# Kernel tuning notes

Hardware: AMD Instinct MI355X
Metric: run time of the kernel (lower is better)

Reference implementation:

```python
import jax, jax.numpy as jnp
import numpy as np

B, H, KVH, S, D, DPE = 16, 128, 1, 4096, 512, 64


def setup_inputs() -> dict:
    key = jax.random.key(0)
    k1, k2, k3, k4 = jax.random.split(key, 4)
    return {
        "q": jax.random.normal(k1, (B, H, D), dtype=jnp.float32),
        "q_pe": jax.random.normal(k2, (B, H, DPE), dtype=jnp.float32),
        "k": jax.random.normal(k3, (B, S, KVH, D), dtype=jnp.float32),
        "k_pe": jax.random.normal(k4, (B, S, KVH, DPE), dtype=jnp.float32),
    }


def reference(q, q_pe, k, k_pe):
    # MLA decode: latent KV cache (k serves as both key-nope part and value),
    # separate rotary-positional path (q_pe, k_pe). kv_head_num groups heads.
    b, h, d = q.shape
    kvh = k.shape[2]
    g = h // kvh  # query heads per latent kv head
    dpe = q_pe.shape[-1]
    scale = 1.0 / jnp.sqrt(jnp.asarray(d + dpe, dtype=q.dtype))
    qg = q.reshape(b, kvh, g, d)          # [b, kvh, g, d]
    qg_pe = q_pe.reshape(b, kvh, g, dpe)  # [b, kvh, g, dpe]
    # scores[b, kvh, g, s] = q . k_latent + q_pe . k_pe
    scores = (jnp.einsum('bkgd,bskd->bkgs', qg, k)
              + jnp.einsum('bkgp,bskp->bkgs', qg_pe, k_pe)) * scale
    p = jax.nn.softmax(scores, axis=-1)
    # value = latent cache (nope dim part)
    out = jnp.einsum('bkgs,bskd->bkgd', p, k)
    return out.reshape(b, h, d)
```

## Files before the change

kernel.cpp:

```cpp
#include <hip/hip_runtime.h>
#include <hip/hip_bf16.h>

typedef __attribute__((ext_vector_type(4))) float  f32x4;
typedef __attribute__((ext_vector_type(8))) short  s16x8;

#define NB_    16
#define NH_    128
#define NS_    4096
#define ND_    512
#define NDPE_  64
#define NCHUNK 16
#define CHUNK_ 256
#define TS_    32
#define NSUB_  8
#define NT_    512

#define KROW_S 584
#define VROW_S 40

#define KBUF_OFF 0
#define VBUF_OFF (TS_ * KROW_S * 2)
#define PBUF_OFF (VBUF_OFF + ND_ * VROW_S * 2)
#define SMEM_BYTES (PBUF_OFF + 8 * 16 * VROW_S * 2)

#define CL2 0.06011229337037348f

__device__ __forceinline__ unsigned short f2bf(float f) {
    unsigned u = __float_as_uint(f);
    u += 0x7FFFu + ((u >> 16) & 1u);
    return (unsigned short)(u >> 16);
}

__global__ __launch_bounds__(NT_, 2) void mla_attn(
    const float* __restrict__ q, const float* __restrict__ q_pe,
    const float* __restrict__ k, const float* __restrict__ k_pe,
    unsigned short* __restrict__ opart, float* __restrict__ mlbuf)
{
    extern __shared__ char smem[];
    unsigned short* kbuf = (unsigned short*)(smem + KBUF_OFF);
    unsigned short* vbuf = (unsigned short*)(smem + VBUF_OFF);
    unsigned short* pbuf = (unsigned short*)(smem + PBUF_OFF);

    const int chunk = blockIdx.x, b = blockIdx.y;
    const int tid = threadIdx.x;
    const int wv  = tid >> 6;
    const int l   = tid & 63;
    const int l16 = l & 15;
    const int lq  = l >> 4;

    f32x4 acc[32];
    #pragma unroll
    for (int i = 0; i < 32; ++i) acc[i] = (f32x4)0.0f;
    float m2[4]   = {-1e30f, -1e30f, -1e30f, -1e30f};
    float lsum[4] = {0.f, 0.f, 0.f, 0.f};

    const int sl   = tid >> 4;
    const int ln16 = tid & 15;

    const float* qrow   = q    + (size_t)(b*NH_ + wv*16 + l16) * ND_;
    const float* qperow = q_pe + (size_t)(b*NH_ + wv*16 + l16) * NDPE_;

    unsigned short* prow = pbuf + wv * 16 * VROW_S;

    for (int t = 0; t < NSUB_; ++t) {
        {
            const int sg = chunk*CHUNK_ + t*TS_ + sl;
            const float* krow   = k    + (size_t)(b*NS_ + sg) * ND_;
            const float* kperow = k_pe + (size_t)(b*NS_ + sg) * NDPE_;
            #pragma unroll
            for (int i = 0; i < 9; ++i) {
                const int d0 = ln16*4 + i*64;
                f32x4 v;
                if (i < 8) v = *(const f32x4*)(krow + d0);
                else       v = *(const f32x4*)(kperow + (d0 - ND_));
                const unsigned short b0 = f2bf(v.x), b1 = f2bf(v.y),
                                     b2 = f2bf(v.z), b3 = f2bf(v.w);
                unsigned* kp = (unsigned*)&kbuf[sl*KROW_S + d0];
                kp[0] = (unsigned)b0 | ((unsigned)b1 << 16);
                kp[1] = (unsigned)b2 | ((unsigned)b3 << 16);
                if (i < 8) {
                    vbuf[(d0+0)*VROW_S + sl] = b0;
                    vbuf[(d0+1)*VROW_S + sl] = b1;
                    vbuf[(d0+2)*VROW_S + sl] = b2;
                    vbuf[(d0+3)*VROW_S + sl] = b3;
                }
            }
        }
        __syncthreads();

        f32x4 sc0 = (f32x4)0.0f, sc1 = (f32x4)0.0f;
        #pragma unroll
        for (int kk = 0; kk < 18; ++kk) {
            const int d0 = kk*32 + lq*8;
            f32x4 qa, qb;
            if (kk < 16) {
                qa = *(const f32x4*)(qrow + d0);
                qb = *(const f32x4*)(qrow + d0 + 4);
            } else {
                qa = *(const f32x4*)(qperow + (d0 - ND_));
                qb = *(const f32x4*)(qperow + (d0 - ND_ + 4));
            }
            s16x8 af;
            {
                union { unsigned u[4]; s16x8 s; } w;
                w.u[0] = (unsigned)f2bf(qa.x) | ((unsigned)f2bf(qa.y) << 16);
                w.u[1] = (unsigned)f2bf(qa.z) | ((unsigned)f2bf(qa.w) << 16);
                w.u[2] = (unsigned)f2bf(qb.x) | ((unsigned)f2bf(qb.y) << 16);
                w.u[3] = (unsigned)f2bf(qb.z) | ((unsigned)f2bf(qb.w) << 16);
                af = w.s;
            }
            const s16x8 bf0 = *(const s16x8*)&kbuf[(l16     )*KROW_S + d0];
            const s16x8 bf1 = *(const s16x8*)&kbuf[(l16 + 16)*KROW_S + d0];
            sc0 = __builtin_amdgcn_mfma_f32_16x16x32_bf16(af, bf0, sc0, 0, 0, 0);
            sc1 = __builtin_amdgcn_mfma_f32_16x16x32_bf16(af, bf1, sc1, 0, 0, 0);
        }

        float alpha[4];
        #pragma unroll
        for (int r = 0; r < 4; ++r) {
            float mx = fmaxf(sc0[r], sc1[r]);
            mx = fmaxf(mx, __shfl_xor(mx, 1));
            mx = fmaxf(mx, __shfl_xor(mx, 2));
            mx = fmaxf(mx, __shfl_xor(mx, 4));
            mx = fmaxf(mx, __shfl_xor(mx, 8));
            const float mn = fmaxf(m2[r], mx * CL2);
            const float al = exp2f(m2[r] - mn);
            const float p0 = exp2f(fmaf(sc0[r], CL2, -mn));
            const float p1 = exp2f(fmaf(sc1[r], CL2, -mn));
            float sm = p0 + p1;
            sm += __shfl_xor(sm, 1);
            sm += __shfl_xor(sm, 2);
            sm += __shfl_xor(sm, 4);
            sm += __shfl_xor(sm, 8);
            lsum[r] = al * lsum[r] + sm;
            m2[r] = mn;
            alpha[r] = al;
            prow[(lq*4 + r)*VROW_S + l16]      = f2bf(p0);
            prow[(lq*4 + r)*VROW_S + 16 + l16] = f2bf(p1);
        }
        #pragma unroll
        for (int nf = 0; nf < 32; ++nf) {
            acc[nf][0] *= alpha[0];
            acc[nf][1] *= alpha[1];
            acc[nf][2] *= alpha[2];
            acc[nf][3] *= alpha[3];
        }
        asm volatile("s_waitcnt lgkmcnt(0)" ::: "memory");
        __builtin_amdgcn_sched_barrier(0);

        const s16x8 pf = *(const s16x8*)&prow[l16*VROW_S + lq*8];
        #pragma unroll
        for (int nf = 0; nf < 32; ++nf) {
            const s16x8 vf = *(const s16x8*)&vbuf[(nf*16 + l16)*VROW_S + lq*8];
            acc[nf] = __builtin_amdgcn_mfma_f32_16x16x32_bf16(pf, vf, acc[nf], 0, 0, 0);
        }
        __syncthreads();
    }

    const size_t obase = (size_t)(b*NCHUNK + chunk) * NH_ * ND_;
    #pragma unroll
    for (int nf = 0; nf < 32; ++nf) {
        #pragma unroll
        for (int r = 0; r < 4; ++r) {
            const int h = wv*16 + lq*4 + r;
            const int d = nf*16 + l16;
            opart[obase + (size_t)h*ND_ + d] = f2bf(acc[nf][r]);
        }
    }
    if (l16 == 0) {
        #pragma unroll
        for (int r = 0; r < 4; ++r) {
            const int h = wv*16 + lq*4 + r;
            const int idx = (b*NCHUNK + chunk)*NH_ + h;
            mlbuf[2*idx]   = m2[r];
            mlbuf[2*idx+1] = lsum[r];
        }
    }
}

__global__ __launch_bounds__(128) void mla_combine(
    const unsigned short* __restrict__ opart, const float* __restrict__ mlbuf,
    float* __restrict__ out)
{
    const int bh = blockIdx.x;
    const int b = bh >> 7, h = bh & 127;
    const int tid = threadIdx.x;

    float mv[NCHUNK], lv[NCHUNK];
    float m = -1e30f;
    #pragma unroll
    for (int c = 0; c < NCHUNK; ++c) {
        const int idx = (b*NCHUNK + c)*NH_ + h;
        mv[c] = mlbuf[2*idx];
        lv[c] = mlbuf[2*idx+1];
        m = fmaxf(m, mv[c]);
    }
    float L = 0.f, w[NCHUNK];
    #pragma unroll
    for (int c = 0; c < NCHUNK; ++c) { w[c] = exp2f(mv[c] - m); L += w[c]*lv[c]; }
    const float inv = 1.0f / L;

    const int d0 = tid * 4;
    float a0 = 0.f, a1 = 0.f, a2 = 0.f, a3 = 0.f;
    #pragma unroll
    for (int c = 0; c < NCHUNK; ++c) {
        const unsigned short* p = opart + (((size_t)(b*NCHUNK + c)*NH_ + h)*ND_ + d0);
        const unsigned u0 = *(const unsigned*)(p);
        const unsigned u1 = *(const unsigned*)(p + 2);
        a0 += w[c] * __uint_as_float((u0 & 0xffffu) << 16);
        a1 += w[c] * __uint_as_float(u0 & 0xffff0000u);
        a2 += w[c] * __uint_as_float((u1 & 0xffffu) << 16);
        a3 += w[c] * __uint_as_float(u1 & 0xffff0000u);
    }
    f32x4 res;
    res.x = a0 * inv; res.y = a1 * inv; res.z = a2 * inv; res.w = a3 * inv;
    *(f32x4*)(out + ((size_t)(b*NH_ + h)*ND_ + d0)) = res;
}

extern "C" void kernel_launch(void* const* d_in, const int* in_sizes, int n_in,
                              void* d_out, int out_size, void* d_ws, size_t ws_size,
                              hipStream_t stream) {
    const float* q    = (const float*)d_in[0];
    const float* q_pe = (const float*)d_in[1];
    const float* k    = (const float*)d_in[2];
    const float* k_pe = (const float*)d_in[3];

    unsigned short* opart = (unsigned short*)d_ws;
    float* mlbuf = (float*)((char*)d_ws + (size_t)NB_*NCHUNK*NH_*ND_*sizeof(unsigned short));

    mla_attn<<<dim3(NCHUNK, NB_), NT_, SMEM_BYTES, stream>>>(q, q_pe, k, k_pe, opart, mlbuf);
    mla_combine<<<NB_*NH_, 128, 0, stream>>>(opart, mlbuf, (float*)d_out);
}
```

Baseline: 87.92 us.

## Double-buffer K/V tiles in LDS and prefetch the next tile into registers

Splits K/V staging into a global load into registers, issued after the QK MFMAs, and an LDS write after the PV MFMAs, with ping-pong LDS buffers. The aim is to hide global-load latency behind compute and to drop one barrier per tile. It also narrows the transposed V row stride to 36 and reads it as two 8-byte loads to change the bank pattern, and switches to the HIP bf16 conversion intrinsics. In exchange it doubles LDS use, which may hurt two-blocks-per-CU occupancy, and adds 36 live registers for the prefetch.

```diff
diff --git a/kernel.cpp b/kernel.cpp
--- a/kernel.cpp
+++ b/kernel.cpp
@@ -3,6 +3,7 @@
 
 typedef __attribute__((ext_vector_type(4))) float  f32x4;
 typedef __attribute__((ext_vector_type(8))) short  s16x8;
+typedef __attribute__((ext_vector_type(4))) short  s16x4;
 
 #define NB_    16
 #define NH_    128
@@ -16,19 +17,55 @@
 #define NT_    512
 
 #define KROW_S 584
-#define VROW_S 40
-
-#define KBUF_OFF 0
-#define VBUF_OFF (TS_ * KROW_S * 2)
-#define PBUF_OFF (VBUF_OFF + ND_ * VROW_S * 2)
-#define SMEM_BYTES (PBUF_OFF + 8 * 16 * VROW_S * 2)
+#define VT_ROW 36
+#define PROW   40
+
+#define KBUF_BYTES (TS_ * KROW_S * 2)
+#define VBUF_BYTES (ND_ * VT_ROW * 2)
+#define VBUF_OFF   (2 * KBUF_BYTES)
+#define PBUF_OFF   (VBUF_OFF + 2 * VBUF_BYTES)
+#define SMEM_BYTES (PBUF_OFF + 8 * 16 * PROW * 2)
 
 #define CL2 0.06011229337037348f
 
-__device__ __forceinline__ unsigned short f2bf(float f) {
-    unsigned u = __float_as_uint(f);
-    u += 0x7FFFu + ((u >> 16) & 1u);
-    return (unsigned short)(u >> 16);
+__device__ __forceinline__ unsigned pk_bf16(float a, float b) {
+    union { __hip_bfloat162 h2; unsigned u; } c;
+    c.h2 = __float22bfloat162_rn(make_float2(a, b));
+    return c.u;
+}
+__device__ __forceinline__ unsigned short bf1(float a) {
+    union { __hip_bfloat16 h; unsigned short u; } c;
+    c.h = __float2bfloat16(a);
+    return c.u;
+}
+
+__device__ __forceinline__ void stage_load(f32x4* R, const float* krow,
+                                           const float* kperow, int ln16) {
+    #pragma unroll
+    for (int i = 0; i < 9; ++i) {
+        const int d0 = ln16 * 4 + i * 64;
+        R[i] = (i < 8) ? *(const f32x4*)(krow + d0)
+                       : *(const f32x4*)(kperow + (d0 - ND_));
+    }
+}
+
+__device__ __forceinline__ void stage_write(const f32x4* R, unsigned short* kb,
+                                            unsigned short* vt, int sl, int ln16) {
+    #pragma unroll
+    for (int i = 0; i < 9; ++i) {
+        const int d0 = ln16 * 4 + i * 64;
+        const f32x4 v = R[i];
+        const unsigned lo = pk_bf16(v.x, v.y);
+        const unsigned hi = pk_bf16(v.z, v.w);
+        unsigned* kp = (unsigned*)&kb[sl * KROW_S + d0];
+        kp[0] = lo; kp[1] = hi;
+        if (i < 8) {
+            vt[(d0 + 0) * VT_ROW + sl] = (unsigned short)(lo & 0xffffu);
+            vt[(d0 + 1) * VT_ROW + sl] = (unsigned short)(lo >> 16);
+            vt[(d0 + 2) * VT_ROW + sl] = (unsigned short)(hi & 0xffffu);
+            vt[(d0 + 3) * VT_ROW + sl] = (unsigned short)(hi >> 16);
+        }
+    }
 }
 
 __global__ __launch_bounds__(NT_, 2) void mla_attn(
@@ -37,7 +74,7 @@
     unsigned short* __restrict__ opart, float* __restrict__ mlbuf)
 {
     extern __shared__ char smem[];
-    unsigned short* kbuf = (unsigned short*)(smem + KBUF_OFF);
+    unsigned short* kbuf = (unsigned short*)(smem);
     unsigned short* vbuf = (unsigned short*)(smem + VBUF_OFF);
     unsigned short* pbuf = (unsigned short*)(smem + PBUF_OFF);
 
@@ -60,33 +97,20 @@
     const float* qrow   = q    + (size_t)(b*NH_ + wv*16 + l16) * ND_;
     const float* qperow = q_pe + (size_t)(b*NH_ + wv*16 + l16) * NDPE_;
 
-    unsigned short* prow = pbuf + wv * 16 * VROW_S;
+    unsigned short* prow = pbuf + wv * 16 * PROW;
+
+    {
+        const int sg = chunk*CHUNK_ + sl;
+        f32x4 R[9];
+        stage_load(R, k + (size_t)(b*NS_ + sg)*ND_, k_pe + (size_t)(b*NS_ + sg)*NDPE_, ln16);
+        stage_write(R, kbuf, vbuf, sl, ln16);
+    }
+    __syncthreads();
 
     for (int t = 0; t < NSUB_; ++t) {
-        {
-            const int sg = chunk*CHUNK_ + t*TS_ + sl;
-            const float* krow   = k    + (size_t)(b*NS_ + sg) * ND_;
-            const float* kperow = k_pe + (size_t)(b*NS_ + sg) * NDPE_;
-            #pragma unroll
-            for (int i = 0; i < 9; ++i) {
-                const int d0 = ln16*4 + i*64;
-                f32x4 v;
-                if (i < 8) v = *(const f32x4*)(krow + d0);
-                else       v = *(const f32x4*)(kperow + (d0 - ND_));
-                const unsigned short b0 = f2bf(v.x), b1 = f2bf(v.y),
-                                     b2 = f2bf(v.z), b3 = f2bf(v.w);
-                unsigned* kp = (unsigned*)&kbuf[sl*KROW_S + d0];
-                kp[0] = (unsigned)b0 | ((unsigned)b1 << 16);
-                kp[1] = (unsigned)b2 | ((unsigned)b3 << 16);
-                if (i < 8) {
-                    vbuf[(d0+0)*VROW_S + sl] = b0;
-                    vbuf[(d0+1)*VROW_S + sl] = b1;
-                    vbuf[(d0+2)*VROW_S + sl] = b2;
-                    vbuf[(d0+3)*VROW_S + sl] = b3;
-                }
-            }
-        }
-        __syncthreads();
+        const int idx = t & 1;
+        const unsigned short* kbc = kbuf + idx * (TS_ * KROW_S);
+        const unsigned short* vtc = vbuf + idx * (ND_ * VT_ROW);
 
         f32x4 sc0 = (f32x4)0.0f, sc1 = (f32x4)0.0f;
         #pragma unroll
@@ -103,16 +127,22 @@
             s16x8 af;
             {
                 union { unsigned u[4]; s16x8 s; } w;
-                w.u[0] = (unsigned)f2bf(qa.x) | ((unsigned)f2bf(qa.y) << 16);
-                w.u[1] = (unsigned)f2bf(qa.z) | ((unsigned)f2bf(qa.w) << 16);
-                w.u[2] = (unsigned)f2bf(qb.x) | ((unsigned)f2bf(qb.y) << 16);
-                w.u[3] = (unsigned)f2bf(qb.z) | ((unsigned)f2bf(qb.w) << 16);
+                w.u[0] = pk_bf16(qa.x, qa.y);
+                w.u[1] = pk_bf16(qa.z, qa.w);
+                w.u[2] = pk_bf16(qb.x, qb.y);
+                w.u[3] = pk_bf16(qb.z, qb.w);
                 af = w.s;
             }
-            const s16x8 bf0 = *(const s16x8*)&kbuf[(l16     )*KROW_S + d0];
-            const s16x8 bf1 = *(const s16x8*)&kbuf[(l16 + 16)*KROW_S + d0];
-            sc0 = __builtin_amdgcn_mfma_f32_16x16x32_bf16(af, bf0, sc0, 0, 0, 0);
-            sc1 = __builtin_amdgcn_mfma_f32_16x16x32_bf16(af, bf1, sc1, 0, 0, 0);
+            const s16x8 bf0 = *(const s16x8*)&kbc[(l16     )*KROW_S + d0];
+            const s16x8 bf1v = *(const s16x8*)&kbc[(l16 + 16)*KROW_S + d0];
+            sc0 = __builtin_amdgcn_mfma_f32_16x16x32_bf16(af, bf0,  sc0, 0, 0, 0);
+            sc1 = __builtin_amdgcn_mfma_f32_16x16x32_bf16(af, bf1v, sc1, 0, 0, 0);
+        }
+
+        f32x4 R[9];
+        if (t + 1 < NSUB_) {
+            const int sg = chunk*CHUNK_ + (t+1)*TS_ + sl;
+            stage_load(R, k + (size_t)(b*NS_ + sg)*ND_, k_pe + (size_t)(b*NS_ + sg)*NDPE_, ln16);
         }
 
         float alpha[4];
@@ -135,8 +165,8 @@
             lsum[r] = al * lsum[r] + sm;
             m2[r] = mn;
             alpha[r] = al;
-            prow[(lq*4 + r)*VROW_S + l16]      = f2bf(p0);
-            prow[(lq*4 + r)*VROW_S + 16 + l16] = f2bf(p1);
+            prow[(lq*4 + r)*PROW + l16]      = bf1(p0);
+            prow[(lq*4 + r)*PROW + 16 + l16] = bf1(p1);
         }
         #pragma unroll
         for (int nf = 0; nf < 32; ++nf) {
@@ -148,11 +178,18 @@
         asm volatile("s_waitcnt lgkmcnt(0)" ::: "memory");
         __builtin_amdgcn_sched_barrier(0);
 
-        const s16x8 pf = *(const s16x8*)&prow[l16*VROW_S + lq*8];
+        const s16x8 pf = *(const s16x8*)&prow[l16*PROW + lq*8];
         #pragma unroll
         for (int nf = 0; nf < 32; ++nf) {
-            const s16x8 vf = *(const s16x8*)&vbuf[(nf*16 + l16)*VROW_S + lq*8];
-            acc[nf] = __builtin_amdgcn_mfma_f32_16x16x32_bf16(pf, vf, acc[nf], 0, 0, 0);
+            const int ro = (nf*16 + l16)*VT_ROW + lq*8;
+            union { s16x4 h[2]; s16x8 v; } u;
+            u.h[0] = *(const s16x4*)&vtc[ro];
+            u.h[1] = *(const s16x4*)&vtc[ro + 4];
+            acc[nf] = __builtin_amdgcn_mfma_f32_16x16x32_bf16(pf, u.v, acc[nf], 0, 0, 0);
+        }
+
+        if (t + 1 < NSUB_) {
+            stage_write(R, kbuf + (idx^1)*(TS_*KROW_S), vbuf + (idx^1)*(ND_*VT_ROW), sl, ln16);
         }
         __syncthreads();
     }
@@ -164,7 +201,7 @@
         for (int r = 0; r < 4; ++r) {
             const int h = wv*16 + lq*4 + r;
             const int d = nf*16 + l16;
-            opart[obase + (size_t)h*ND_ + d] = f2bf(acc[nf][r]);
+            opart[obase + (size_t)h*ND_ + d] = bf1(acc[nf][r]);
         }
     }
     if (l16 == 0) {
```

After: 116.7 us. +32.8%, slower.
